# Kernel tuning notes

Measured on AMD Instinct MI355X. Metric: run time of the kernel, lower is better.

## Reference

```python
import jax, jax.numpy as jnp
import numpy as np

N_DIM = 16
E_DIM = 16
M_DIM = 16
HIDDEN = 64
N_EDGE = 1_600_000
N_NODE = 100_000


def setup_inputs() -> dict:
    key = jax.random.key(0)
    k1, k2, k3, k4, k5, k6, k7 = jax.random.split(key, 7)
    index_v = jax.random.randint(k1, (N_EDGE,), 0, N_NODE, dtype=jnp.int32)
    h_w = jax.random.normal(k2, (N_EDGE, N_DIM), dtype=jnp.float32)
    e_vw = jax.random.normal(k3, (N_EDGE, E_DIM), dtype=jnp.float32)
    # NNet params: Linear(e_dim, hidden) -> ReLU -> Linear(hidden, n_dim*m_dim)
    s1 = 1.0 / np.sqrt(E_DIM)
    s2 = 1.0 / np.sqrt(HIDDEN)
    W1 = jax.random.uniform(k4, (E_DIM, HIDDEN), jnp.float32, -s1, s1)
    b1 = jax.random.uniform(k5, (HIDDEN,), jnp.float32, -s1, s1)
    W2 = jax.random.uniform(k6, (HIDDEN, N_DIM * M_DIM), jnp.float32, -s2, s2)
    b2 = jax.random.uniform(k7, (N_DIM * M_DIM,), jnp.float32, -s2, s2)
    return {"index_v": index_v, "h_w": h_w, "e_vw": e_vw, "n_node": N_NODE,
            "W1": W1, "b1": b1, "W2": W2, "b2": b2}


def reference(index_v, h_w, e_vw, n_node, W1, b1, W2, b2):
    # Edge MLP: [n_edge, e_dim] -> [n_edge, n_dim*m_dim]
    hid = jax.nn.relu(e_vw @ W1 + b1)
    A_vw = (hid @ W2 + b2).reshape(-1, M_DIM, N_DIM)  # [n_edge, m_dim, n_dim]
    # Per-edge matvec: bmm(A_vw, h_w[:, :, None]) -> [n_edge, m_dim]
    m_vw = jnp.einsum("emn,en->em", A_vw, h_w)
    # Scatter-add messages to target nodes: [n_node, m_dim]
    m_v = jax.ops.segment_sum(m_vw, index_v, num_segments=n_node)
    return m_v
```

## Files before the change

kernel.cpp:

```cpp
#include <hip/hip_runtime.h>
#include <stdint.h>

typedef __bf16 bf16x8 __attribute__((ext_vector_type(8)));
typedef float  f32x4  __attribute__((ext_vector_type(4)));
typedef float  fvec4  __attribute__((ext_vector_type(4)));
typedef float  f32x2  __attribute__((ext_vector_type(2)));
typedef int    i32x4  __attribute__((ext_vector_type(4)));

#define EDIM   16
#define HIDDEN 64
#define MDIM   16
#define NDIM   16
#define KCHUNKS 32
#define NREP   8
#define WPB    8

__device__ __forceinline__ uint32_t pack_trunc(float x, float y) {
    return __builtin_amdgcn_perm(__builtin_bit_cast(uint32_t, x),
                                 __builtin_bit_cast(uint32_t, y),
                                 0x03020706u);
}

__device__ __forceinline__ uint16_t f32_to_bf16_rne(float f) {
    uint32_t u = __builtin_bit_cast(uint32_t, f);
    u += 0x7FFFu + ((u >> 16) & 1u);
    return (uint16_t)(u >> 16);
}

__device__ __forceinline__ bf16x8 u4_as_bf16x8(uint32_t a, uint32_t b,
                                               uint32_t c, uint32_t d) {
    union { uint32_t u[4]; bf16x8 v; } x;
    x.u[0] = a; x.u[1] = b; x.u[2] = c; x.u[3] = d;
    return x.v;
}

__device__ __forceinline__ f32x2 pk_mul_bcast(f32x2 a, f32x2 b) {
    f32x2 d;
    asm("v_pk_mul_f32 %0, %1, %2 op_sel_hi:[0,1]" : "=v"(d) : "v"(a), "v"(b));
    return d;
}

__device__ __forceinline__ void atomic_add_s(const float* base, uint32_t off,
                                             float v) {
    asm volatile("global_atomic_add_f32 %0, %1, %2"
                 :: "v"(off), "v"(v), "s"(base) : "memory");
}

__device__ __forceinline__ void load_eh(const float* p, uint32_t ro,
                                        fvec4& a, fvec4& b) {
    const fvec4* pp = (const fvec4*)(p + ro);
    a = __builtin_nontemporal_load(pp);
    b = __builtin_nontemporal_load(pp + 1);
}

__device__ __forceinline__ i32x4 load_idx4(const int* __restrict__ idx,
                                           int r, int n_edge, bool full) {
    i32x4 v;
    if (full) {
        v = __builtin_nontemporal_load((const i32x4*)(idx + r));
    } else {
        v.x = __builtin_nontemporal_load(idx + min(r + 0, n_edge - 1));
        v.y = __builtin_nontemporal_load(idx + min(r + 1, n_edge - 1));
        v.z = __builtin_nontemporal_load(idx + min(r + 2, n_edge - 1));
        v.w = __builtin_nontemporal_load(idx + min(r + 3, n_edge - 1));
    }
    return v;
}

__device__ __forceinline__ void hid_stage(fvec4 ea, fvec4 eb, int q,
                                          const bf16x8* w1f, ushort* hidWr) {
    uint32_t au0 = pack_trunc(ea.x, ea.y);
    uint32_t au1 = pack_trunc(ea.z, ea.w);
    uint32_t au2 = pack_trunc(eb.x, eb.y);
    uint32_t au3 = pack_trunc(eb.z, eb.w);
    if (q == 2) { au0 = 0x00003F80u; au1 = au2 = au3 = 0; }
    else if (q == 3) { au0 = au1 = au2 = au3 = 0; }
    bf16x8 av = u4_as_bf16x8(au0, au1, au2, au3);
    #pragma unroll
    for (int nt = 0; nt < 4; nt++) {
        f32x4 hc = {0.f, 0.f, 0.f, 0.f};
        hc = __builtin_amdgcn_mfma_f32_16x16x32_bf16(av, w1f[nt], hc, 0, 0, 0);
        uint32_t lo = pack_trunc(fmaxf(hc[0], 0.f), fmaxf(hc[1], 0.f));
        uint32_t hi = pack_trunc(fmaxf(hc[2], 0.f), fmaxf(hc[3], 0.f));
        *(uint2*)(hidWr + nt * 256) = make_uint2(lo, hi);
    }
}

__global__ __launch_bounds__(512, 4) void msg_mfma32(
    const int*   __restrict__ idx,
    const float* __restrict__ h_w,
    const float* __restrict__ e_vw,
    const float* __restrict__ W1,
    const float* __restrict__ b1,
    const float* __restrict__ W2,
    const float* __restrict__ b2,
    float*       __restrict__ outb,
    int n_edge, int rep_stride)
{
    __align__(16) __shared__ ushort sB[KCHUNKS * 512];
    __align__(16) __shared__ ushort sHid[WPB * 2 * 1024];

    const int tid = threadIdx.x;

    const int xcd = __builtin_amdgcn_s_getreg(6164) & (NREP - 1);
    const float* out = outb + (size_t)xcd * (size_t)rep_stride;

    for (int t = tid; t < KCHUNKS * 512; t += 512) {
        int c = t >> 9, r = t & 511;
        int qq = r >> 7, m = (r >> 3) & 15, j = r & 7;
        int k = 2 * c + (qq >> 1);
        int n = ((qq & 1) << 3) + j;
        sB[t] = f32_to_bf16_rne(W2[k * 256 + m * 16 + n]);
    }

    const int lane = tid & 63;
    const int q    = lane >> 4;
    const int col  = lane & 15;
    const int w    = tid >> 6;

    uint32_t w1u[4][4];
    #pragma unroll
    for (int nt = 0; nt < 4; nt++) {
        #pragma unroll
        for (int d = 0; d < 4; d++) w1u[nt][d] = 0;
        #pragma unroll
        for (int j = 0; j < 8; j++) {
            int k = q * 8 + j;
            float v = 0.f;
            if (k < 16)       v = W1[k * 64 + nt * 16 + col];
            else if (k == 16) v = b1[nt * 16 + col];
            w1u[nt][j >> 1] |= ((uint32_t)f32_to_bf16_rne(v)) << ((j & 1) * 16);
        }
    }

    uint32_t b2u[4] = {0, 0, 0, 0};
    if (q < 2) {
        const float* bp = b2 + col * 16 + q * 8;
        #pragma unroll
        for (int j = 0; j < 8; j++)
            b2u[j >> 1] |= ((uint32_t)f32_to_bf16_rne(bp[j])) << ((j & 1) * 16);
    }
    __syncthreads();

    bf16x8 w1f[4];
    #pragma unroll
    for (int nt = 0; nt < 4; nt++)
        w1f[nt] = u4_as_bf16x8(w1u[nt][0], w1u[nt][1], w1u[nt][2], w1u[nt][3]);
    const bf16x8 b2f = u4_as_bf16x8(b2u[0], b2u[1], b2u[2], b2u[3]);

    const int nhalf = (q & 1) << 3;
    const int ntile = (n_edge + 31) >> 5;
    const int wave_id = blockIdx.x * WPB + w;
    const int wstride = gridDim.x * WPB;
    if (wave_id >= ntile) return;

    const ushort* hidRd0 = &sHid[(w * 2 + 0) * 1024 + (q >> 1) * 16 + col];
    const ushort* hidRd1 = hidRd0 + 1024;
    ushort*       hidWr0 = &sHid[(w * 2 + 0) * 1024 + col * 16 + q * 4];
    ushort*       hidWr1 = hidWr0 + 1024;
    const ushort* bRd    = &sB[q * 128 + col * 8];
    const uint32_t col4  = (uint32_t)col * 4u;

    int t = wave_id;
    fvec4 e0, e1, e2, e3, h0, h1, h2, h3; i32x4 nd0, nd1; bool full;
    {
        int rbase = t * 32;
        full = (rbase + 32 <= n_edge);
        int row0 = full ? (rbase + col)      : min(rbase + col,      n_edge - 1);
        int row1 = full ? (rbase + 16 + col) : min(rbase + 16 + col, n_edge - 1);
        uint32_t ro0 = (uint32_t)row0 * 16u + (uint32_t)nhalf;
        uint32_t ro1 = (uint32_t)row1 * 16u + (uint32_t)nhalf;
        load_eh(e_vw, ro0, e0, e1);
        load_eh(e_vw, ro1, e2, e3);
        load_eh(h_w,  ro0, h0, h1);
        load_eh(h_w,  ro1, h2, h3);
        nd0 = load_idx4(idx, rbase + q * 4,      n_edge, full);
        nd1 = load_idx4(idx, rbase + 16 + q * 4, n_edge, full);
    }

    while (true) {
        int tn = t + wstride;
        bool have_next = (tn < ntile);

        hid_stage(e0, e1, q, w1f, hidWr0);
        hid_stage(e2, e3, q, w1f, hidWr1);

        bool nfull = false;
        if (have_next) {
            int rbase = tn * 32;
            nfull = (rbase + 32 <= n_edge);
            int row0 = nfull ? (rbase + col)      : min(rbase + col,      n_edge - 1);
            int row1 = nfull ? (rbase + 16 + col) : min(rbase + 16 + col, n_edge - 1);
            load_eh(e_vw, (uint32_t)row0 * 16u + (uint32_t)nhalf, e0, e1);
            load_eh(e_vw, (uint32_t)row1 * 16u + (uint32_t)nhalf, e2, e3);
        }

        f32x2 hp0; hp0.x = h0.x; hp0.y = h0.y;
        f32x2 hp1; hp1.x = h0.z; hp1.y = h0.w;
        f32x2 hp2; hp2.x = h1.x; hp2.y = h1.y;
        f32x2 hp3; hp3.x = h1.z; hp3.y = h1.w;
        f32x2 hq0; hq0.x = h2.x; hq0.y = h2.y;
        f32x2 hq1; hq1.x = h2.z; hq1.y = h2.w;
        f32x2 hq2; hq2.x = h3.x; hq2.y = h3.y;
        f32x2 hq3; hq3.x = h3.z; hq3.y = h3.w;

        f32x4 acc0 = {0.f, 0.f, 0.f, 0.f};
        f32x4 acc1 = {0.f, 0.f, 0.f, 0.f};
        {
            bf16x8 af0 = u4_as_bf16x8(pack_trunc(hp0.x, hp0.y), pack_trunc(hp1.x, hp1.y),
                                      pack_trunc(hp2.x, hp2.y), pack_trunc(hp3.x, hp3.y));
            acc0 = __builtin_amdgcn_mfma_f32_16x16x32_bf16(af0, b2f, acc0, 0, 0, 0);
            bf16x8 af1 = u4_as_bf16x8(pack_trunc(hq0.x, hq0.y), pack_trunc(hq1.x, hq1.y),
                                      pack_trunc(hq2.x, hq2.y), pack_trunc(hq3.x, hq3.y));
            acc1 = __builtin_amdgcn_mfma_f32_16x16x32_bf16(af1, b2f, acc1, 0, 0, 0);
        }

        f32x2 hkA = {0.f, 0.f}, hkB = {0.f, 0.f};
        #pragma unroll
        for (int c = 0; c < KCHUNKS; c++) {
            bf16x8 bfb = *(const bf16x8*)(bRd + c * 512);
            {
                hkA[0] = __builtin_bit_cast(float,
                             ((uint32_t)hidRd0[c * 32]) << 16);
                f32x2 p0 = pk_mul_bcast(hkA, hp0);
                f32x2 p1 = pk_mul_bcast(hkA, hp1);
                f32x2 p2 = pk_mul_bcast(hkA, hp2);
                f32x2 p3 = pk_mul_bcast(hkA, hp3);
                bf16x8 af = u4_as_bf16x8(pack_trunc(p0.x, p0.y), pack_trunc(p1.x, p1.y),
                                         pack_trunc(p2.x, p2.y), pack_trunc(p3.x, p3.y));
                acc0 = __builtin_amdgcn_mfma_f32_16x16x32_bf16(af, bfb, acc0, 0, 0, 0);
            }
            {
                hkB[0] = __builtin_bit_cast(float,
                             ((uint32_t)hidRd1[c * 32]) << 16);
                f32x2 p0 = pk_mul_bcast(hkB, hq0);
                f32x2 p1 = pk_mul_bcast(hkB, hq1);
                f32x2 p2 = pk_mul_bcast(hkB, hq2);
                f32x2 p3 = pk_mul_bcast(hkB, hq3);
                bf16x8 af = u4_as_bf16x8(pack_trunc(p0.x, p0.y), pack_trunc(p1.x, p1.y),
                                         pack_trunc(p2.x, p2.y), pack_trunc(p3.x, p3.y));
                acc1 = __builtin_amdgcn_mfma_f32_16x16x32_bf16(af, bfb, acc1, 0, 0, 0);
            }
        }

        i32x4 ndn0, ndn1;
        if (have_next) {
            int rbase = tn * 32;
            int row0 = nfull ? (rbase + col)      : min(rbase + col,      n_edge - 1);
            int row1 = nfull ? (rbase + 16 + col) : min(rbase + 16 + col, n_edge - 1);
            load_eh(h_w, (uint32_t)row0 * 16u + (uint32_t)nhalf, h0, h1);
            load_eh(h_w, (uint32_t)row1 * 16u + (uint32_t)nhalf, h2, h3);
            ndn0 = load_idx4(idx, rbase + q * 4,      n_edge, nfull);
            ndn1 = load_idx4(idx, rbase + 16 + q * 4, n_edge, nfull);
        }

        if (full) {
            atomic_add_s(out, (uint32_t)nd0.x * 64u + col4, acc0[0]);
            atomic_add_s(out, (uint32_t)nd0.y * 64u + col4, acc0[1]);
            atomic_add_s(out, (uint32_t)nd0.z * 64u + col4, acc0[2]);
            atomic_add_s(out, (uint32_t)nd0.w * 64u + col4, acc0[3]);
            atomic_add_s(out, (uint32_t)nd1.x * 64u + col4, acc1[0]);
            atomic_add_s(out, (uint32_t)nd1.y * 64u + col4, acc1[1]);
            atomic_add_s(out, (uint32_t)nd1.z * 64u + col4, acc1[2]);
            atomic_add_s(out, (uint32_t)nd1.w * 64u + col4, acc1[3]);
        } else {
            int r0 = t * 32 + q * 4;
            int r1 = r0 + 16;
            if (r0 + 0 < n_edge) atomic_add_s(out, (uint32_t)nd0.x * 64u + col4, acc0[0]);
            if (r0 + 1 < n_edge) atomic_add_s(out, (uint32_t)nd0.y * 64u + col4, acc0[1]);
            if (r0 + 2 < n_edge) atomic_add_s(out, (uint32_t)nd0.z * 64u + col4, acc0[2]);
            if (r0 + 3 < n_edge) atomic_add_s(out, (uint32_t)nd0.w * 64u + col4, acc0[3]);
            if (r1 + 0 < n_edge) atomic_add_s(out, (uint32_t)nd1.x * 64u + col4, acc1[0]);
            if (r1 + 1 < n_edge) atomic_add_s(out, (uint32_t)nd1.y * 64u + col4, acc1[1]);
            if (r1 + 2 < n_edge) atomic_add_s(out, (uint32_t)nd1.z * 64u + col4, acc1[2]);
            if (r1 + 3 < n_edge) atomic_add_s(out, (uint32_t)nd1.w * 64u + col4, acc1[3]);
        }

        if (!have_next) break;
        t = tn; full = nfull; nd0 = ndn0; nd1 = ndn1;
    }
}

__global__ __launch_bounds__(512, 6) void msg_mfma_legacy(
    const int*   __restrict__ idx,
    const float* __restrict__ h_w,
    const float* __restrict__ e_vw,
    const float* __restrict__ W1,
    const float* __restrict__ b1,
    const float* __restrict__ W2,
    const float* __restrict__ b2,
    float*       __restrict__ out,
    int n_edge)
{
    __align__(16) __shared__ ushort sB[KCHUNKS * 512];
    __align__(16) __shared__ ushort sHid[WPB * 64 * 16];
    const int tid = threadIdx.x;
    for (int t = tid; t < KCHUNKS * 512; t += 512) {
        int c = t >> 9, r = t & 511;
        int qq = r >> 7, m = (r >> 3) & 15, j = r & 7;
        int k = 2 * c + (qq >> 1);
        int n = ((qq & 1) << 3) + j;
        sB[t] = f32_to_bf16_rne(W2[k * 256 + m * 16 + n]);
    }
    const int lane = tid & 63, q = lane >> 4, col = lane & 15, w = tid >> 6;
    uint32_t w1u[4][4];
    #pragma unroll
    for (int nt = 0; nt < 4; nt++) {
        #pragma unroll
        for (int d = 0; d < 4; d++) w1u[nt][d] = 0;
        #pragma unroll
        for (int j = 0; j < 8; j++) {
            int k = q * 8 + j;
            float v = 0.f;
            if (k < 16)       v = W1[k * 64 + nt * 16 + col];
            else if (k == 16) v = b1[nt * 16 + col];
            w1u[nt][j >> 1] |= ((uint32_t)f32_to_bf16_rne(v)) << ((j & 1) * 16);
        }
    }
    uint32_t b2u[4] = {0, 0, 0, 0};
    if (q < 2) {
        const float* bp = b2 + col * 16 + q * 8;
        #pragma unroll
        for (int j = 0; j < 8; j++)
            b2u[j >> 1] |= ((uint32_t)f32_to_bf16_rne(bp[j])) << ((j & 1) * 16);
    }
    __syncthreads();
    bf16x8 w1f[4];
    #pragma unroll
    for (int nt = 0; nt < 4; nt++)
        w1f[nt] = u4_as_bf16x8(w1u[nt][0], w1u[nt][1], w1u[nt][2], w1u[nt][3]);
    const bf16x8 b2f = u4_as_bf16x8(b2u[0], b2u[1], b2u[2], b2u[3]);
    const int nhalf = (q & 1) << 3;
    const int ntile = (n_edge + 15) >> 4;
    int t = blockIdx.x * WPB + w;
    const int wstride = gridDim.x * WPB;
    const ushort* hidRd = &sHid[w * 1024 + (q >> 1) * 16 + col];
    ushort*       hidWr = &sHid[w * 1024 + col * 16 + q * 4];
    const ushort* bRd   = &sB[q * 128 + col * 8];
    for (; t < ntile; t += wstride) {
        int row = min(t * 16 + col, n_edge - 1);
        const fvec4* ep = (const fvec4*)(e_vw + (size_t)row * 16 + nhalf);
        fvec4 e0 = ep[0], e1 = ep[1];
        const fvec4* hpp = (const fvec4*)(h_w + (size_t)row * 16 + nhalf);
        fvec4 h0 = hpp[0], h1 = hpp[1];
        int r0 = t * 16 + q * 4;
        int4 nd;
        nd.x = idx[min(r0 + 0, n_edge - 1)];
        nd.y = idx[min(r0 + 1, n_edge - 1)];
        nd.z = idx[min(r0 + 2, n_edge - 1)];
        nd.w = idx[min(r0 + 3, n_edge - 1)];
        hid_stage(e0, e1, q, w1f, hidWr);
        float hf[8] = {h0.x, h0.y, h0.z, h0.w, h1.x, h1.y, h1.z, h1.w};
        f32x4 acc = {0.f, 0.f, 0.f, 0.f};
        {
            uint32_t a0 = pack_trunc(hf[0], hf[1]);
            uint32_t a1 = pack_trunc(hf[2], hf[3]);
            uint32_t a2 = pack_trunc(hf[4], hf[5]);
            uint32_t a3 = pack_trunc(hf[6], hf[7]);
            acc = __builtin_amdgcn_mfma_f32_16x16x32_bf16(
                u4_as_bf16x8(a0, a1, a2, a3), b2f, acc, 0, 0, 0);
        }
        #pragma unroll
        for (int c = 0; c < KCHUNKS; c++) {
            uint32_t hku = ((uint32_t)hidRd[c * 32]) << 16;
            float hk = __builtin_bit_cast(float, hku);
            uint32_t a0 = pack_trunc(hk * hf[0], hk * hf[1]);
            uint32_t a1 = pack_trunc(hk * hf[2], hk * hf[3]);
            uint32_t a2 = pack_trunc(hk * hf[4], hk * hf[5]);
            uint32_t a3 = pack_trunc(hk * hf[6], hk * hf[7]);
            bf16x8 bfb = *(const bf16x8*)(bRd + c * 512);
            acc = __builtin_amdgcn_mfma_f32_16x16x32_bf16(
                u4_as_bf16x8(a0, a1, a2, a3), bfb, acc, 0, 0, 0);
        }
        if (r0 + 0 < n_edge) atomicAdd(out + (size_t)nd.x * 16 + col, acc[0]);
        if (r0 + 1 < n_edge) atomicAdd(out + (size_t)nd.y * 16 + col, acc[1]);
        if (r0 + 2 < n_edge) atomicAdd(out + (size_t)nd.z * 16 + col, acc[2]);
        if (r0 + 3 < n_edge) atomicAdd(out + (size_t)nd.w * 16 + col, acc[3]);
    }
}

__global__ void merge_rep(const fvec4* __restrict__ rep,
                          fvec4* __restrict__ out, int n4, int stride4)
{
    int i = blockIdx.x * blockDim.x + threadIdx.x;
    if (i >= n4) return;
    fvec4 s = rep[i];
    #pragma unroll
    for (int r = 1; r < NREP; r++)
        s += rep[(size_t)r * stride4 + i];
    out[i] = s;
}

extern "C" void kernel_launch(void* const* d_in, const int* in_sizes, int n_in,
                              void* d_out, int out_size, void* d_ws, size_t ws_size,
                              hipStream_t stream) {
    const int*   idx  = (const int*)  d_in[0];
    const float* h_w  = (const float*)d_in[1];
    const float* e_vw = (const float*)d_in[2];
    const float* W1   = (const float*)d_in[4];
    const float* b1   = (const float*)d_in[5];
    const float* W2   = (const float*)d_in[6];
    const float* b2   = (const float*)d_in[7];
    float* out = (float*)d_out;
    const int n_edge = in_sizes[0];

    const size_t out_floats = (size_t)out_size;
    const size_t need = (size_t)NREP * out_floats * sizeof(float);

    if (ws_size >= need && (out_floats & 3) == 0) {
        float* rep = (float*)d_ws;
        (void)hipMemsetAsync(rep, 0, need, stream);
        msg_mfma32<<<512, 512, 0, stream>>>(idx, h_w, e_vw, W1, b1, W2, b2,
                                            rep, n_edge, (int)out_floats);
        const int n4 = (int)(out_floats >> 2);
        const int mblocks = (n4 + 255) / 256;
        merge_rep<<<mblocks, 256, 0, stream>>>((const fvec4*)rep, (fvec4*)out,
                                               n4, n4);
    } else {
        (void)hipMemsetAsync(out, 0, out_floats * sizeof(float), stream);
        msg_mfma_legacy<<<1536, 512, 0, stream>>>(idx, h_w, e_vw, W1, b1, W2,
                                                  b2, out, n_edge);
    }
}
```

Before: 314.4 us.

## Switch edge MLP path to fp16 MFMA with packed f16 multiplies and transposed hidden layout

Converts the main kernel from bf16 to fp16 MFMA. Per-chunk products become packed v_pk_mul_f16 operations, replacing f32 packed multiplies followed by truncation. The hidden activations are stored transposed in a padded LDS layout, so each lane reads its 32 hidden values with a few vector loads instead of 32 scalar loads. Occupancy is raised to 6 blocks per CU with a 768-block grid. fp16 has narrower range than bf16, so large products could overflow.

```diff
diff --git a/kernel.cpp b/kernel.cpp
--- a/kernel.cpp
+++ b/kernel.cpp
@@ -1,11 +1,11 @@
 #include <hip/hip_runtime.h>
 #include <stdint.h>
 
-typedef __bf16 bf16x8 __attribute__((ext_vector_type(8)));
-typedef float  f32x4  __attribute__((ext_vector_type(4)));
-typedef float  fvec4  __attribute__((ext_vector_type(4)));
-typedef float  f32x2  __attribute__((ext_vector_type(2)));
-typedef int    i32x4  __attribute__((ext_vector_type(4)));
+typedef __bf16    bf16x8 __attribute__((ext_vector_type(8)));
+typedef _Float16  f16x8  __attribute__((ext_vector_type(8)));
+typedef float     f32x4  __attribute__((ext_vector_type(4)));
+typedef float     fvec4  __attribute__((ext_vector_type(4)));
+typedef int       i32x4  __attribute__((ext_vector_type(4)));
 
 #define EDIM   16
 #define HIDDEN 64
@@ -14,30 +14,49 @@
 #define KCHUNKS 32
 #define NREP   8
 #define WPB    8
+#define HROW   36
+#define HPBLK  (16 * HROW)
+#define HGRP   (2 * HPBLK)
+
+__device__ __forceinline__ ushort f16bits(float v) {
+    return __builtin_bit_cast(ushort, (_Float16)v);
+}
+__device__ __forceinline__ uint32_t cvt_pk_f16(float x, float y) {
+    return __builtin_bit_cast(uint32_t, __builtin_amdgcn_cvt_pkrtz(x, y));
+}
+__device__ __forceinline__ f16x8 u4_as_f16x8(uint32_t a, uint32_t b,
+                                             uint32_t c, uint32_t d) {
+    union { uint32_t u[4]; f16x8 v; } x;
+    x.u[0] = a; x.u[1] = b; x.u[2] = c; x.u[3] = d;
+    return x.v;
+}
+template<int HALF>
+__device__ __forceinline__ uint32_t pkmul16(uint32_t hk, uint32_t h2) {
+    uint32_t d;
+    if (HALF)
+        asm("v_pk_mul_f16 %0, %1, %2 op_sel:[1,0] op_sel_hi:[1,1]"
+            : "=v"(d) : "v"(hk), "v"(h2));
+    else
+        asm("v_pk_mul_f16 %0, %1, %2 op_sel:[0,0] op_sel_hi:[0,1]"
+            : "=v"(d) : "v"(hk), "v"(h2));
+    return d;
+}
 
 __device__ __forceinline__ uint32_t pack_trunc(float x, float y) {
     return __builtin_amdgcn_perm(__builtin_bit_cast(uint32_t, x),
                                  __builtin_bit_cast(uint32_t, y),
                                  0x03020706u);
 }
-
 __device__ __forceinline__ uint16_t f32_to_bf16_rne(float f) {
     uint32_t u = __builtin_bit_cast(uint32_t, f);
     u += 0x7FFFu + ((u >> 16) & 1u);
     return (uint16_t)(u >> 16);
 }
-
 __device__ __forceinline__ bf16x8 u4_as_bf16x8(uint32_t a, uint32_t b,
                                                uint32_t c, uint32_t d) {
     union { uint32_t u[4]; bf16x8 v; } x;
     x.u[0] = a; x.u[1] = b; x.u[2] = c; x.u[3] = d;
     return x.v;
-}
-
-__device__ __forceinline__ f32x2 pk_mul_bcast(f32x2 a, f32x2 b) {
-    f32x2 d;
-    asm("v_pk_mul_f32 %0, %1, %2 op_sel_hi:[0,1]" : "=v"(d) : "v"(a), "v"(b));
-    return d;
 }
 
 __device__ __forceinline__ void atomic_add_s(const float* base, uint32_t off,
@@ -67,26 +86,27 @@
     return v;
 }
 
-__device__ __forceinline__ void hid_stage(fvec4 ea, fvec4 eb, int q,
-                                          const bf16x8* w1f, ushort* hidWr) {
-    uint32_t au0 = pack_trunc(ea.x, ea.y);
-    uint32_t au1 = pack_trunc(ea.z, ea.w);
-    uint32_t au2 = pack_trunc(eb.x, eb.y);
-    uint32_t au3 = pack_trunc(eb.z, eb.w);
-    if (q == 2) { au0 = 0x00003F80u; au1 = au2 = au3 = 0; }
+__device__ __forceinline__ void hid_stage_f16(fvec4 ea, fvec4 eb, int q,
+                                              const f16x8* w1f,
+                                              ushort* wrBase) {
+    uint32_t au0 = cvt_pk_f16(ea.x, ea.y);
+    uint32_t au1 = cvt_pk_f16(ea.z, ea.w);
+    uint32_t au2 = cvt_pk_f16(eb.x, eb.y);
+    uint32_t au3 = cvt_pk_f16(eb.z, eb.w);
+    if (q == 2) { au0 = 0x00003C00u; au1 = au2 = au3 = 0; }
     else if (q == 3) { au0 = au1 = au2 = au3 = 0; }
-    bf16x8 av = u4_as_bf16x8(au0, au1, au2, au3);
+    f16x8 av = u4_as_f16x8(au0, au1, au2, au3);
     #pragma unroll
     for (int nt = 0; nt < 4; nt++) {
         f32x4 hc = {0.f, 0.f, 0.f, 0.f};
-        hc = __builtin_amdgcn_mfma_f32_16x16x32_bf16(av, w1f[nt], hc, 0, 0, 0);
-        uint32_t lo = pack_trunc(fmaxf(hc[0], 0.f), fmaxf(hc[1], 0.f));
-        uint32_t hi = pack_trunc(fmaxf(hc[2], 0.f), fmaxf(hc[3], 0.f));
-        *(uint2*)(hidWr + nt * 256) = make_uint2(lo, hi);
-    }
-}
-
-__global__ __launch_bounds__(512, 4) void msg_mfma32(
+        hc = __builtin_amdgcn_mfma_f32_16x16x32_f16(av, w1f[nt], hc, 0, 0, 0);
+        #pragma unroll
+        for (int i = 0; i < 4; i++)
+            wrBase[i * HROW + nt * 8] = f16bits(fmaxf(hc[i], 0.f));
+    }
+}
+
+__global__ __launch_bounds__(512, 6) void msg_mfma32_f16(
     const int*   __restrict__ idx,
     const float* __restrict__ h_w,
     const float* __restrict__ e_vw,
@@ -98,7 +118,7 @@
     int n_edge, int rep_stride)
 {
     __align__(16) __shared__ ushort sB[KCHUNKS * 512];
-    __align__(16) __shared__ ushort sHid[WPB * 2 * 1024];
+    __align__(16) __shared__ ushort sHidT[WPB * HGRP];
 
     const int tid = threadIdx.x;
 
@@ -110,7 +130,7 @@
         int qq = r >> 7, m = (r >> 3) & 15, j = r & 7;
         int k = 2 * c + (qq >> 1);
         int n = ((qq & 1) << 3) + j;
-        sB[t] = f32_to_bf16_rne(W2[k * 256 + m * 16 + n]);
+        sB[t] = f16bits(W2[k * 256 + m * 16 + n]);
     }
 
     const int lane = tid & 63;
@@ -129,24 +149,23 @@
             float v = 0.f;
             if (k < 16)       v = W1[k * 64 + nt * 16 + col];
             else if (k == 16) v = b1[nt * 16 + col];
-            w1u[nt][j >> 1] |= ((uint32_t)f32_to_bf16_rne(v)) << ((j & 1) * 16);
-        }
-    }
-
+            w1u[nt][j >> 1] |= ((uint32_t)f16bits(v)) << ((j & 1) * 16);
+        }
+    }
     uint32_t b2u[4] = {0, 0, 0, 0};
     if (q < 2) {
         const float* bp = b2 + col * 16 + q * 8;
         #pragma unroll
         for (int j = 0; j < 8; j++)
-            b2u[j >> 1] |= ((uint32_t)f32_to_bf16_rne(bp[j])) << ((j & 1) * 16);
+            b2u[j >> 1] |= ((uint32_t)f16bits(bp[j])) << ((j & 1) * 16);
     }
     __syncthreads();
 
-    bf16x8 w1f[4];
+    f16x8 w1f[4];
     #pragma unroll
     for (int nt = 0; nt < 4; nt++)
-        w1f[nt] = u4_as_bf16x8(w1u[nt][0], w1u[nt][1], w1u[nt][2], w1u[nt][3]);
-    const bf16x8 b2f = u4_as_bf16x8(b2u[0], b2u[1], b2u[2], b2u[3]);
+        w1f[nt] = u4_as_f16x8(w1u[nt][0], w1u[nt][1], w1u[nt][2], w1u[nt][3]);
+    const f16x8 b2f = u4_as_f16x8(b2u[0], b2u[1], b2u[2], b2u[3]);
 
     const int nhalf = (q & 1) << 3;
     const int ntile = (n_edge + 31) >> 5;
@@ -154,12 +173,10 @@
     const int wstride = gridDim.x * WPB;
     if (wave_id >= ntile) return;
 
-    const ushort* hidRd0 = &sHid[(w * 2 + 0) * 1024 + (q >> 1) * 16 + col];
-    const ushort* hidRd1 = hidRd0 + 1024;
-    ushort*       hidWr0 = &sHid[(w * 2 + 0) * 1024 + col * 16 + q * 4];
-    ushort*       hidWr1 = hidWr0 + 1024;
-    const ushort* bRd    = &sB[q * 128 + col * 8];
-    const uint32_t col4  = (uint32_t)col * 4u;
+    ushort* hWr = &sHidT[w * HGRP + (col & 1) * HPBLK + (q * 4) * HROW + (col >> 1)];
+    const ushort* hRd = &sHidT[w * HGRP + (q >> 1) * HPBLK + col * HROW];
+    const ushort* bRd = &sB[q * 128 + col * 8];
+    const uint32_t col4 = (uint32_t)col * 4u;
 
     int t = wave_id;
     fvec4 e0, e1, e2, e3, h0, h1, h2, h3; i32x4 nd0, nd1; bool full;
@@ -182,8 +199,20 @@
         int tn = t + wstride;
         bool have_next = (tn < ntile);
 
-        hid_stage(e0, e1, q, w1f, hidWr0);
-        hid_stage(e2, e3, q, w1f, hidWr1);
+        hid_stage_f16(e0, e1, q, w1f, hWr);
+        uint32_t hv0[16];
+        #pragma unroll
+        for (int j = 0; j < 8; j++) {
+            uint2 t2 = *(const uint2*)(hRd + j * 4);
+            hv0[2 * j] = t2.x; hv0[2 * j + 1] = t2.y;
+        }
+        hid_stage_f16(e2, e3, q, w1f, hWr);
+        uint32_t hv1[16];
+        #pragma unroll
+        for (int j = 0; j < 8; j++) {
+            uint2 t2 = *(const uint2*)(hRd + j * 4);
+            hv1[2 * j] = t2.x; hv1[2 * j + 1] = t2.y;
+        }
 
         bool nfull = false;
         if (have_next) {
@@ -195,51 +224,37 @@
             load_eh(e_vw, (uint32_t)row1 * 16u + (uint32_t)nhalf, e2, e3);
         }
 
-        f32x2 hp0; hp0.x = h0.x; hp0.y = h0.y;
-        f32x2 hp1; hp1.x = h0.z; hp1.y = h0.w;
-        f32x2 hp2; hp2.x = h1.x; hp2.y = h1.y;
-        f32x2 hp3; hp3.x = h1.z; hp3.y = h1.w;
-        f32x2 hq0; hq0.x = h2.x; hq0.y = h2.y;
-        f32x2 hq1; hq1.x = h2.z; hq1.y = h2.w;
-        f32x2 hq2; hq2.x = h3.x; hq2.y = h3.y;
-        f32x2 hq3; hq3.x = h3.z; hq3.y = h3.w;
+        uint32_t hF0 = cvt_pk_f16(h0.x, h0.y), hF1 = cvt_pk_f16(h0.z, h0.w);
+        uint32_t hF2 = cvt_pk_f16(h1.x, h1.y), hF3 = cvt_pk_f16(h1.z, h1.w);
+        uint32_t hG0 = cvt_pk_f16(h2.x, h2.y), hG1 = cvt_pk_f16(h2.z, h2.w);
+        uint32_t hG2 = cvt_pk_f16(h3.x, h3.y), hG3 = cvt_pk_f16(h3.z, h3.w);
 
         f32x4 acc0 = {0.f, 0.f, 0.f, 0.f};
         f32x4 acc1 = {0.f, 0.f, 0.f, 0.f};
-        {
-            bf16x8 af0 = u4_as_bf16x8(pack_trunc(hp0.x, hp0.y), pack_trunc(hp1.x, hp1.y),
-                                      pack_trunc(hp2.x, hp2.y), pack_trunc(hp3.x, hp3.y));
-            acc0 = __builtin_amdgcn_mfma_f32_16x16x32_bf16(af0, b2f, acc0, 0, 0, 0);
-            bf16x8 af1 = u4_as_bf16x8(pack_trunc(hq0.x, hq0.y), pack_trunc(hq1.x, hq1.y),
-                                      pack_trunc(hq2.x, hq2.y), pack_trunc(hq3.x, hq3.y));
-            acc1 = __builtin_amdgcn_mfma_f32_16x16x32_bf16(af1, b2f, acc1, 0, 0, 0);
-        }
-
-        f32x2 hkA = {0.f, 0.f}, hkB = {0.f, 0.f};
-        #pragma unroll
-        for (int c = 0; c < KCHUNKS; c++) {
-            bf16x8 bfb = *(const bf16x8*)(bRd + c * 512);
+        acc0 = __builtin_amdgcn_mfma_f32_16x16x32_f16(
+                   u4_as_f16x8(hF0, hF1, hF2, hF3), b2f, acc0, 0, 0, 0);
+        acc1 = __builtin_amdgcn_mfma_f32_16x16x32_f16(
+                   u4_as_f16x8(hG0, hG1, hG2, hG3), b2f, acc1, 0, 0, 0);
+
+        #pragma unroll
+        for (int d = 0; d < 16; d++) {
             {
-                hkA[0] = __builtin_bit_cast(float,
-                             ((uint32_t)hidRd0[c * 32]) << 16);
-                f32x2 p0 = pk_mul_bcast(hkA, hp0);
-                f32x2 p1 = pk_mul_bcast(hkA, hp1);
-                f32x2 p2 = pk_mul_bcast(hkA, hp2);
-                f32x2 p3 = pk_mul_bcast(hkA, hp3);
-                bf16x8 af = u4_as_bf16x8(pack_trunc(p0.x, p0.y), pack_trunc(p1.x, p1.y),
-                                         pack_trunc(p2.x, p2.y), pack_trunc(p3.x, p3.y));
-                acc0 = __builtin_amdgcn_mfma_f32_16x16x32_bf16(af, bfb, acc0, 0, 0, 0);
+                f16x8 bfb = *(const f16x8*)(bRd + (2 * d) * 512);
+                f16x8 a0 = u4_as_f16x8(pkmul16<0>(hv0[d], hF0), pkmul16<0>(hv0[d], hF1),
+                                       pkmul16<0>(hv0[d], hF2), pkmul16<0>(hv0[d], hF3));
+                acc0 = __builtin_amdgcn_mfma_f32_16x16x32_f16(a0, bfb, acc0, 0, 0, 0);
+                f16x8 a1 = u4_as_f16x8(pkmul16<0>(hv1[d], hG0), pkmul16<0>(hv1[d], hG1),
+                                       pkmul16<0>(hv1[d], hG2), pkmul16<0>(hv1[d], hG3));
+                acc1 = __builtin_amdgcn_mfma_f32_16x16x32_f16(a1, bfb, acc1, 0, 0, 0);
             }
             {
-                hkB[0] = __builtin_bit_cast(float,
-                             ((uint32_t)hidRd1[c * 32]) << 16);
-                f32x2 p0 = pk_mul_bcast(hkB, hq0);
-                f32x2 p1 = pk_mul_bcast(hkB, hq1);
-                f32x2 p2 = pk_mul_bcast(hkB, hq2);
-                f32x2 p3 = pk_mul_bcast(hkB, hq3);
-                bf16x8 af = u4_as_bf16x8(pack_trunc(p0.x, p0.y), pack_trunc(p1.x, p1.y),
-                                         pack_trunc(p2.x, p2.y), pack_trunc(p3.x, p3.y));
-                acc1 = __builtin_amdgcn_mfma_f32_16x16x32_bf16(af, bfb, acc1, 0, 0, 0);
+                f16x8 bfb = *(const f16x8*)(bRd + (2 * d + 1) * 512);
+                f16x8 a0 = u4_as_f16x8(pkmul16<1>(hv0[d], hF0), pkmul16<1>(hv0[d], hF1),
+                                       pkmul16<1>(hv0[d], hF2), pkmul16<1>(hv0[d], hF3));
+                acc0 = __builtin_amdgcn_mfma_f32_16x16x32_f16(a0, bfb, acc0, 0, 0, 0);
+                f16x8 a1 = u4_as_f16x8(pkmul16<1>(hv1[d], hG0), pkmul16<1>(hv1[d], hG1),
+                                       pkmul16<1>(hv1[d], hG2), pkmul16<1>(hv1[d], hG3));
+                acc1 = __builtin_amdgcn_mfma_f32_16x16x32_f16(a1, bfb, acc1, 0, 0, 0);
             }
         }
 
@@ -278,6 +293,25 @@
 
         if (!have_next) break;
         t = tn; full = nfull; nd0 = ndn0; nd1 = ndn1;
+    }
+}
+
+__device__ __forceinline__ void hid_stage_bf16(fvec4 ea, fvec4 eb, int q,
+                                               const bf16x8* w1f, ushort* hidWr) {
+    uint32_t au0 = pack_trunc(ea.x, ea.y);
+    uint32_t au1 = pack_trunc(ea.z, ea.w);
+    uint32_t au2 = pack_trunc(eb.x, eb.y);
+    uint32_t au3 = pack_trunc(eb.z, eb.w);
+    if (q == 2) { au0 = 0x00003F80u; au1 = au2 = au3 = 0; }
+    else if (q == 3) { au0 = au1 = au2 = au3 = 0; }
+    bf16x8 av = u4_as_bf16x8(au0, au1, au2, au3);
+    #pragma unroll
+    for (int nt = 0; nt < 4; nt++) {
+        f32x4 hc = {0.f, 0.f, 0.f, 0.f};
+        hc = __builtin_amdgcn_mfma_f32_16x16x32_bf16(av, w1f[nt], hc, 0, 0, 0);
+        uint32_t lo = pack_trunc(fmaxf(hc[0], 0.f), fmaxf(hc[1], 0.f));
+        uint32_t hi = pack_trunc(fmaxf(hc[2], 0.f), fmaxf(hc[3], 0.f));
+        *(uint2*)(hidWr + nt * 256) = make_uint2(lo, hi);
     }
 }
 
@@ -349,7 +383,7 @@
         nd.y = idx[min(r0 + 1, n_edge - 1)];
         nd.z = idx[min(r0 + 2, n_edge - 1)];
         nd.w = idx[min(r0 + 3, n_edge - 1)];
-        hid_stage(e0, e1, q, w1f, hidWr);
+        hid_stage_bf16(e0, e1, q, w1f, hidWr);
         float hf[8] = {h0.x, h0.y, h0.z, h0.w, h1.x, h1.y, h1.z, h1.w};
         f32x4 acc = {0.f, 0.f, 0.f, 0.f};
         {
@@ -410,8 +444,8 @@
     if (ws_size >= need && (out_floats & 3) == 0) {
         float* rep = (float*)d_ws;
         (void)hipMemsetAsync(rep, 0, need, stream);
-        msg_mfma32<<<512, 512, 0, stream>>>(idx, h_w, e_vw, W1, b1, W2, b2,
-                                            rep, n_edge, (int)out_floats);
+        msg_mfma32_f16<<<768, 512, 0, stream>>>(idx, h_w, e_vw, W1, b1, W2, b2,
+                                                rep, n_edge, (int)out_floats);
         const int n4 = (int)(out_floats >> 2);
         const int mblocks = (n4 + 255) / 256;
         merge_rep<<<mblocks, 256, 0, stream>>>((const fvec4*)rep, (fvec4*)out,
```

Result: slower. 505.4 us (+60.7%).
